# Performance work log

Measured on AMD Instinct MI355X. Metric: run time of the kernel, lower is better.

The kernel has to match this reference:

```python
import jax, jax.numpy as jnp
import numpy as np
import math

B, S, DM, H, F = 2, 2048, 1024, 16, 192  # F = head_dim init arg; per-head dim = F // 3
DH = F // 3
MAX_BIAS = 8.0


def _get_slopes(n):
    # faithful to ALiBiBias._get_slopes
    def pow2(n):
        start = 2.0 ** (-(2.0 ** (-(math.log2(n) - 3))))
        return [start * start ** i for i in range(n)]
    if math.log2(n).is_integer():
        return pow2(n)
    cp2 = 2 ** math.floor(math.log2(n))
    return pow2(cp2) + _get_slopes(2 * cp2)[0::2][: n - cp2]


def _rope_sin_cos(seq_len, dim):
    inv_freq = 1.0 / (10000.0 ** (jnp.arange(0, dim, 2, dtype=jnp.float32) / dim))
    freqs = jnp.outer(jnp.arange(seq_len, dtype=jnp.float32), inv_freq)  # [S, dim/2]
    # repeat(sin[:,None,:],2,axis=1).reshape(S,-1) == concat([sin,sin],-1)
    sin = jnp.concatenate([jnp.sin(freqs), jnp.sin(freqs)], axis=-1)  # [S, dim]
    cos = jnp.concatenate([jnp.cos(freqs), jnp.cos(freqs)], axis=-1)
    return sin, cos


def _rotate_half(x):
    x1, x2 = jnp.split(x, 2, axis=-1)
    return jnp.concatenate([-x2, x1], axis=-1)


def setup_inputs() -> dict:
    key = jax.random.key(0)
    kx, kq, ko = jax.random.split(key, 3)
    x = jax.random.normal(kx, (B, S, DM), dtype=jnp.float32)
    w_qkv = jax.random.normal(kq, (DM, H, F), dtype=jnp.float32) * (1.0 / math.sqrt(DM))
    b_qkv = jnp.zeros((H, F), dtype=jnp.float32)
    w_out = jax.random.normal(ko, (H, DH, DM), dtype=jnp.float32) * (1.0 / math.sqrt(H * DH))
    b_out = jnp.zeros((DM,), dtype=jnp.float32)
    return {"x": x, "w_qkv": w_qkv, "b_qkv": b_qkv, "w_out": w_out, "b_out": b_out}


def reference(x, w_qkv, b_qkv, w_out, b_out):
    b, s, dm = x.shape
    h, f = w_qkv.shape[1], w_qkv.shape[2]
    dh = f // 3
    # fused QKV projection: [B,S,H,F], then 3-way split on the feature axis
    qkv = jnp.einsum('bsd,dhf->bshf', x, w_qkv) + b_qkv
    q, k, v = jnp.split(qkv, 3, axis=-1)  # each [B,S,H,DH]
    # RoPE (rotate_half convention), broadcast over heads
    sin, cos = _rope_sin_cos(s, dh)
    sin, cos = sin[:, None, :], cos[:, None, :]  # [S,1,DH]
    q = q * cos + _rotate_half(q) * sin
    k = k * cos + _rotate_half(k) * sin
    # [B,H,S,DH]
    q = q.transpose(0, 2, 1, 3)
    k = k.transpose(0, 2, 1, 3)
    v = v.transpose(0, 2, 1, 3)
    # scores scaled by sqrt(head_dim init arg), as in the original non-flash path
    scores = jnp.einsum('bhqd,bhkd->bhqk', q, k) / jnp.sqrt(jnp.float32(f))
    # ALiBi bias
    slopes = jnp.asarray(_get_slopes(h), dtype=jnp.float32)  # [H]
    pos = jnp.arange(s, dtype=jnp.float32)
    rel = pos[None, :] - pos[:, None]  # j - i
    rel = jnp.where(rel > 0, 0.0, rel)
    alibi = rel[None, :, :] * slopes[:, None, None] * MAX_BIAS  # [H,S,S]
    scores = scores + alibi[None]  # [B,H,S,S]
    # causal mask
    causal = jnp.tril(jnp.ones((s, s), dtype=jnp.float32))
    scores = jnp.where(causal == 0, -1e9, scores)
    weights = jax.nn.softmax(scores, axis=-1)
    attn = jnp.einsum('bhqk,bhkd->bhqd', weights, v).transpose(0, 2, 1, 3)  # [B,S,H,DH]
    return jnp.einsum('bshd,hdm->bsm', attn, w_out) + b_out
```

## Files before the change

### kernel.cpp

```cpp
#include <hip/hip_runtime.h>
#include <math.h>

static constexpr int B_  = 2;
static constexpr int S_  = 2048;
static constexpr int H_  = 16;
static constexpr int DH_ = 64;
static constexpr float QSCALE2_ = 0.104117589f;
static constexpr float C8L2_    = 11.5415603f;

typedef __attribute__((ext_vector_type(8))) short short8;
typedef __attribute__((ext_vector_type(4))) float floatx4;

__device__ __forceinline__ float bf2f(unsigned short u) {
    union { unsigned int i; float f; } c; c.i = ((unsigned int)u) << 16; return c.f;
}
__device__ __forceinline__ unsigned short f2bf(float f) {
    union { float f; unsigned int i; } c; c.f = f;
    unsigned int x = c.i;
    unsigned int r = (x + 0x7fffu + ((x >> 16) & 1u)) >> 16;
    if ((x & 0x7f800000u) == 0x7f800000u) r = x >> 16;
    return (unsigned short)r;
}
__device__ __forceinline__ void load_lds16(const unsigned short* g, unsigned short* l) {
    __builtin_amdgcn_global_load_lds(
        (const __attribute__((address_space(1))) unsigned int*)g,
        (__attribute__((address_space(3))) unsigned int*)l, 16, 0, 0);
}

__global__ __launch_bounds__(256) void cvt_x(
    const float* __restrict__ in, unsigned short* __restrict__ out)
{
    const int i = blockIdx.x * 256 + threadIdx.x;
    const float4 v = reinterpret_cast<const float4*>(in)[i];
    ushort4 r;
    r.x = f2bf(v.x); r.y = f2bf(v.y); r.z = f2bf(v.z); r.w = f2bf(v.w);
    reinterpret_cast<ushort4*>(out)[i] = r;
}

template<int NN>
__global__ __launch_bounds__(256) void transcvt(
    const float* __restrict__ in, unsigned short* __restrict__ out)
{
    __shared__ float t[32][33];
    const int n0 = blockIdx.x * 32;
    const int k0 = blockIdx.y * 32;
    const int tn = threadIdx.x & 31, tk = threadIdx.x >> 5;
    #pragma unroll
    for (int i = 0; i < 4; ++i)
        t[tk + 8 * i][tn] = in[(size_t)(k0 + tk + 8 * i) * NN + n0 + tn];
    __syncthreads();
    #pragma unroll
    for (int i = 0; i < 4; ++i)
        out[(size_t)(n0 + tk + 8 * i) * 1024 + k0 + tn] = f2bf(t[tn][tk + 8 * i]);
}

template<int NW, int MODE>
__global__ __launch_bounds__(256) void gemm_mfma(
    const unsigned short* __restrict__ A, const unsigned short* __restrict__ BT,
    const float* __restrict__ bias,
    unsigned short* __restrict__ O0, unsigned short* __restrict__ O1,
    unsigned short* __restrict__ O2, float* __restrict__ Of)
{
    __shared__ unsigned short As[128 * 32];
    __shared__ unsigned short Bs[128 * 32];

    const int tid  = threadIdx.x;
    const int wave = tid >> 6;
    const int lane = tid & 63;
    const int quad = lane >> 4;
    const int lm   = lane & 15;
    const int wm = (wave >> 1) * 64;
    const int wn = (wave & 1) * 64;
    const int n0 = blockIdx.x * 128;
    const int m0 = blockIdx.y * 128;

    floatx4 acc[4][4] = {};

    const int sr = lane >> 2;
    const int sc = lane & 3;

    for (int k0 = 0; k0 < 1024; k0 += 32) {
        #pragma unroll
        for (int rep = 0; rep < 2; ++rep) {
            const int r = wave * 32 + rep * 16;
            load_lds16(A  + (size_t)(m0 + r + sr) * 1024 + k0 + sc * 8, &As[r * 32]);
            load_lds16(BT + (size_t)(n0 + r + sr) * 1024 + k0 + sc * 8, &Bs[r * 32]);
        }
        __syncthreads();
        short8 af[4], bf[4];
        #pragma unroll
        for (int i = 0; i < 4; ++i) {
            af[i] = *reinterpret_cast<const short8*>(&As[(wm + i * 16 + lm) * 32 + quad * 8]);
            bf[i] = *reinterpret_cast<const short8*>(&Bs[(wn + i * 16 + lm) * 32 + quad * 8]);
        }
        #pragma unroll
        for (int mi = 0; mi < 4; ++mi)
            #pragma unroll
            for (int ni = 0; ni < 4; ++ni)
                acc[mi][ni] = __builtin_amdgcn_mfma_f32_16x16x32_bf16(
                    af[mi], bf[ni], acc[mi][ni], 0, 0, 0);
        __syncthreads();
    }

    if (MODE == 1) {
        #pragma unroll
        for (int ni = 0; ni < 4; ++ni) {
            const int gn = n0 + wn + ni * 16 + lm;
            const float b = bias[gn];
            #pragma unroll
            for (int mi = 0; mi < 4; ++mi) {
                const int gm = m0 + wm + mi * 16 + quad * 4;
                #pragma unroll
                for (int r = 0; r < 4; ++r)
                    Of[(size_t)(gm + r) * 1024 + gn] = acc[mi][ni][r] + b;
            }
        }
    } else {
        const int nbase = n0 + wn;
        const int h   = nbase / 192;
        const int sec = (nbase - h * 192) >> 6;
        float bia[4];
        #pragma unroll
        for (int ni = 0; ni < 4; ++ni) bia[ni] = bias[nbase + ni * 16 + lm];
        unsigned short* Out = (sec == 0) ? O0 : ((sec == 1) ? O1 : O2);

        if (sec == 2) {
            #pragma unroll
            for (int mi = 0; mi < 4; ++mi) {
                const int m  = m0 + wm + mi * 16 + quad * 4;
                const int bb = m >> 11;
                const int s  = m & (S_ - 1);
                const size_t rowb = (size_t)(bb * H_ + h) * DH_;
                #pragma unroll
                for (int ni = 0; ni < 4; ++ni) {
                    const int d = ni * 16 + lm;
                    ushort4 w;
                    w.x = f2bf(acc[mi][ni][0] + bia[ni]);
                    w.y = f2bf(acc[mi][ni][1] + bia[ni]);
                    w.z = f2bf(acc[mi][ni][2] + bia[ni]);
                    w.w = f2bf(acc[mi][ni][3] + bia[ni]);
                    *reinterpret_cast<ushort4*>(&Out[(rowb + d) * S_ + s]) = w;
                }
            }
        } else {
            const float qscale = (sec == 0) ? QSCALE2_ : 1.0f;
            const float nlf = -13.287712379549449f / 32.0f;
            const float invf0 = exp2f((float)lm * nlf);
            const float invf1 = exp2f((float)(lm + 16) * nlf);
            #pragma unroll
            for (int mi = 0; mi < 4; ++mi) {
                #pragma unroll
                for (int r = 0; r < 4; ++r) {
                    const int m  = m0 + wm + mi * 16 + quad * 4 + r;
                    const int bb = m >> 11;
                    const int s  = m & (S_ - 1);
                    const size_t obase = ((size_t)(bb * H_ + h) * S_ + s) * DH_;
                    const float a0 = (float)s * invf0, a1 = (float)s * invf1;
                    const float sn0 = __sinf(a0), cs0 = __cosf(a0);
                    const float sn1 = __sinf(a1), cs1 = __cosf(a1);
                    #pragma unroll
                    for (int ni = 0; ni < 4; ++ni) {
                        const int d = ni * 16 + lm;
                        const float v = acc[mi][ni][r]     + bia[ni];
                        const float p = acc[mi][ni ^ 2][r] + bia[ni ^ 2];
                        const float cs = (ni & 1) ? cs1 : cs0;
                        const float sn = (ni & 1) ? sn1 : sn0;
                        float res = (d < 32) ? (v * cs - p * sn) : (v * cs + p * sn);
                        Out[obase + d] = f2bf(res * qscale);
                    }
                }
            }
        }
    }
}

static constexpr int KST = 68;
static constexpr int PST = 68;

__global__ __launch_bounds__(256) void flash_mfma(
    const unsigned short* __restrict__ Q, const unsigned short* __restrict__ K,
    const unsigned short* __restrict__ VT, unsigned short* __restrict__ Ao)
{
    __shared__ unsigned short Ks[2][64 * KST];
    __shared__ unsigned short VTs[2][64 * KST];
    __shared__ unsigned short Ps[4][16 * PST];

    const int bi = blockIdx.x;
    const int bh = bi & 31;
    const int pr = bi >> 5;
    const int h  = bh & 15;
    const int b  = bh >> 4;
    const int tid  = threadIdx.x;
    const int wave = tid >> 6;
    const int lane = tid & 63;
    const int quad = lane >> 4;
    const int lm   = lane & 15;
    const int srow = tid >> 2;
    const int sc8  = tid & 3;

    const unsigned short* Kg  = K  + (size_t)bh * S_ * DH_;
    const unsigned short* VTg = VT + (size_t)bh * DH_ * S_;

    const float slope2 = exp2f(-0.5f * (float)(h + 1)) * (8.0f * 1.44269504f);
    const float d64 = 64.0f * slope2;

    int   koff[4];
    float alb[4];
    #pragma unroll
    for (int t = 0; t < 4; ++t) {
        koff[t] = t * 16 + quad * 4 - wave * 16 - lm;
        alb[t]  = (float)koff[t] * slope2 - C8L2_;
    }

    unsigned short* Pw = &Ps[wave][0];

    for (int ph = 0; ph < 2; ++ph) {
        const int qt = ph ? pr : 31 - pr;

        const unsigned short* Qrow =
            Q + ((size_t)bh * S_ + (size_t)(qt * 64 + wave * 16 + lm)) * DH_;
        const short8 aq0 = *reinterpret_cast<const short8*>(Qrow + quad * 8);
        const short8 aq1 = *reinterpret_cast<const short8*>(Qrow + 32 + quad * 8);

        float crk[4];
        #pragma unroll
        for (int r = 0; r < 4; ++r)
            crk[r] = (float)r * slope2 - (float)qt * d64;

        float l_one = 0.0f;
        floatx4 acc_o[4] = {};

        short8 ka, kb, va, vb;
        {
            const unsigned short* kr = Kg + (size_t)srow * DH_ + sc8 * 8;
            ka = *reinterpret_cast<const short8*>(kr);
            kb = *reinterpret_cast<const short8*>(kr + 32);
            const unsigned short* vr = VTg + (size_t)srow * S_ + sc8 * 8;
            va = *reinterpret_cast<const short8*>(vr);
            vb = *reinterpret_cast<const short8*>(vr + 32);
        }
        *reinterpret_cast<short8*>(&Ks[0][srow * KST + sc8 * 8])       = ka;
        *reinterpret_cast<short8*>(&Ks[0][srow * KST + sc8 * 8 + 32])  = kb;
        *reinterpret_cast<short8*>(&VTs[0][srow * KST + sc8 * 8])      = va;
        *reinterpret_cast<short8*>(&VTs[0][srow * KST + sc8 * 8 + 32]) = vb;
        if (qt > 0) {
            const unsigned short* kr = Kg + (size_t)(64 + srow) * DH_ + sc8 * 8;
            ka = *reinterpret_cast<const short8*>(kr);
            kb = *reinterpret_cast<const short8*>(kr + 32);
            const unsigned short* vr = VTg + (size_t)srow * S_ + 64 + sc8 * 8;
            va = *reinterpret_cast<const short8*>(vr);
            vb = *reinterpret_cast<const short8*>(vr + 32);
        }
        __syncthreads();

        for (int kt = 0; kt <= qt; ++kt) {
            const int cur = kt & 1;

            if (kt < qt) {
                const int nxt = cur ^ 1;
                *reinterpret_cast<short8*>(&Ks[nxt][srow * KST + sc8 * 8])       = ka;
                *reinterpret_cast<short8*>(&Ks[nxt][srow * KST + sc8 * 8 + 32])  = kb;
                *reinterpret_cast<short8*>(&VTs[nxt][srow * KST + sc8 * 8])      = va;
                *reinterpret_cast<short8*>(&VTs[nxt][srow * KST + sc8 * 8 + 32]) = vb;
                if (kt + 1 < qt) {
                    const unsigned short* kr =
                        Kg + (size_t)((kt + 2) * 64 + srow) * DH_ + sc8 * 8;
                    ka = *reinterpret_cast<const short8*>(kr);
                    kb = *reinterpret_cast<const short8*>(kr + 32);
                    const unsigned short* vr =
                        VTg + (size_t)srow * S_ + (kt + 2) * 64 + sc8 * 8;
                    va = *reinterpret_cast<const short8*>(vr);
                    vb = *reinterpret_cast<const short8*>(vr + 32);
                }
            }

            floatx4 sacc[4] = {};
            #pragma unroll
            for (int t = 0; t < 4; ++t) {
                const short8 k0 = *reinterpret_cast<const short8*>(&Ks[cur][(t * 16 + lm) * KST + quad * 8]);
                const short8 k1 = *reinterpret_cast<const short8*>(&Ks[cur][(t * 16 + lm) * KST + 32 + quad * 8]);
                sacc[t] = __builtin_amdgcn_mfma_f32_16x16x32_bf16(k0, aq0, sacc[t], 0, 0, 0);
                sacc[t] = __builtin_amdgcn_mfma_f32_16x16x32_bf16(k1, aq1, sacc[t], 0, 0, 0);
            }

            const bool diag = (kt == qt);
            #pragma unroll
            for (int t = 0; t < 4; ++t) {
                float p[4];
                #pragma unroll
                for (int r = 0; r < 4; ++r) {
                    const float x = (sacc[t][r] + alb[t]) + crk[r];
                    float e;
                    asm("v_exp_f32 %0, %1" : "=v"(e) : "v"(x));
                    if (diag && (koff[t] + r) > 0) e = 0.0f;
                    p[r] = e;
                }
                l_one += (p[0] + p[1]) + (p[2] + p[3]);
                unsigned int lo, hi;
                asm("v_cvt_pk_bf16_f32 %0, %1, %2" : "=v"(lo) : "v"(p[0]), "v"(p[1]));
                asm("v_cvt_pk_bf16_f32 %0, %1, %2" : "=v"(hi) : "v"(p[2]), "v"(p[3]));
                uint2 w; w.x = lo; w.y = hi;
                *reinterpret_cast<uint2*>(&Pw[lm * PST + t * 16 + quad * 4]) = w;
            }
            #pragma unroll
            for (int r = 0; r < 4; ++r) crk[r] += d64;

            const short8 ap0 = *reinterpret_cast<const short8*>(&Pw[lm * PST + quad * 8]);
            const short8 ap1 = *reinterpret_cast<const short8*>(&Pw[lm * PST + 32 + quad * 8]);
            #pragma unroll
            for (int t = 0; t < 4; ++t) {
                const short8 v0 = *reinterpret_cast<const short8*>(&VTs[cur][(t * 16 + lm) * KST + quad * 8]);
                const short8 v1 = *reinterpret_cast<const short8*>(&VTs[cur][(t * 16 + lm) * KST + 32 + quad * 8]);
                acc_o[t] = __builtin_amdgcn_mfma_f32_16x16x32_bf16(ap0, v0, acc_o[t], 0, 0, 0);
                acc_o[t] = __builtin_amdgcn_mfma_f32_16x16x32_bf16(ap1, v1, acc_o[t], 0, 0, 0);
            }
            __syncthreads();
        }

        l_one += __shfl_xor(l_one, 16);
        l_one += __shfl_xor(l_one, 32);
        #pragma unroll
        for (int r = 0; r < 4; ++r) {
            const float lr = __shfl(l_one, quad * 4 + r);
            const float inv_l = 1.0f / lr;
            const int s = qt * 64 + wave * 16 + quad * 4 + r;
            const size_t obase = ((size_t)(b * S_ + s) * H_ + h) * DH_;
            #pragma unroll
            for (int t = 0; t < 4; ++t)
                Ao[obase + t * 16 + lm] = f2bf(acc_o[t][r] * inv_l);
        }
    }
}

extern "C" void kernel_launch(void* const* d_in, const int* in_sizes, int n_in,
                              void* d_out, int out_size, void* d_ws, size_t ws_size,
                              hipStream_t stream)
{
    const float *x = nullptr, *w_qkv = nullptr, *b_qkv = nullptr,
                *w_out = nullptr, *b_out = nullptr;
    for (int i = 0; i < n_in; ++i) {
        switch (in_sizes[i]) {
            case 4194304: x     = (const float*)d_in[i]; break;
            case 3145728: w_qkv = (const float*)d_in[i]; break;
            case 3072:    b_qkv = (const float*)d_in[i]; break;
            case 1048576: w_out = (const float*)d_in[i]; break;
            case 1024:    b_out = (const float*)d_in[i]; break;
        }
    }
    if (!x)     x     = (const float*)d_in[0];
    if (!w_qkv) w_qkv = (const float*)d_in[1];
    if (!b_qkv) b_qkv = (const float*)d_in[2];
    if (!w_out) w_out = (const float*)d_in[3];
    if (!b_out) b_out = (const float*)d_in[4];

    float* out = (float*)d_out;
    unsigned short* ws16 = (unsigned short*)d_ws;

    unsigned short* xb     = ws16;
    unsigned short* wqkvT  = ws16 + (size_t)4194304;
    unsigned short* woutT  = ws16 + (size_t)7340032;
    unsigned short* Qb     = ws16 + (size_t)8388608;
    unsigned short* Kb     = ws16 + (size_t)12582912;
    unsigned short* Vb     = ws16 + (size_t)16777216;
    unsigned short* Aob    = ws16 + (size_t)20971520;

    cvt_x<<<4096, 256, 0, stream>>>(x, xb);
    transcvt<3072><<<dim3(96, 32), 256, 0, stream>>>(w_qkv, wqkvT);
    transcvt<1024><<<dim3(32, 32), 256, 0, stream>>>(w_out, woutT);

    gemm_mfma<3072, 0><<<dim3(24, 32), 256, 0, stream>>>(
        xb, wqkvT, b_qkv, Qb, Kb, Vb, nullptr);
    flash_mfma<<<dim3(512), 256, 0, stream>>>(Qb, Kb, Vb, Aob);
    gemm_mfma<1024, 1><<<dim3(8, 32), 256, 0, stream>>>(
        Aob, woutT, b_out, nullptr, nullptr, nullptr, out);
}
```

Baseline: 199.4 us.

## Merge prep kernels, shrink output GEMM tile, add MFMA priority hints in flash

```diff
diff --git a/kernel.cpp b/kernel.cpp
--- a/kernel.cpp
+++ b/kernel.cpp
@@ -27,23 +27,31 @@
         (__attribute__((address_space(3))) unsigned int*)l, 16, 0, 0);
 }
 
-__global__ __launch_bounds__(256) void cvt_x(
-    const float* __restrict__ in, unsigned short* __restrict__ out)
-{
-    const int i = blockIdx.x * 256 + threadIdx.x;
-    const float4 v = reinterpret_cast<const float4*>(in)[i];
-    ushort4 r;
-    r.x = f2bf(v.x); r.y = f2bf(v.y); r.z = f2bf(v.z); r.w = f2bf(v.w);
-    reinterpret_cast<ushort4*>(out)[i] = r;
-}
-
-template<int NN>
-__global__ __launch_bounds__(256) void transcvt(
-    const float* __restrict__ in, unsigned short* __restrict__ out)
+__global__ __launch_bounds__(256) void prep(
+    const float* __restrict__ x,     unsigned short* __restrict__ xb,
+    const float* __restrict__ w_qkv, unsigned short* __restrict__ wqkvT,
+    const float* __restrict__ w_out, unsigned short* __restrict__ woutT)
 {
     __shared__ float t[32][33];
-    const int n0 = blockIdx.x * 32;
-    const int k0 = blockIdx.y * 32;
+    const int bid = blockIdx.x;
+    if (bid < 4096) {
+        const int i = bid * 256 + threadIdx.x;
+        const float4 v = reinterpret_cast<const float4*>(x)[i];
+        ushort4 r;
+        r.x = f2bf(v.x); r.y = f2bf(v.y); r.z = f2bf(v.z); r.w = f2bf(v.w);
+        reinterpret_cast<ushort4*>(xb)[i] = r;
+        return;
+    }
+    const float* in; unsigned short* out; int NN, bx, by;
+    if (bid < 7168) {
+        in = w_qkv; out = wqkvT; NN = 3072;
+        const int b2 = bid - 4096; bx = b2 % 96; by = b2 / 96;
+    } else {
+        in = w_out; out = woutT; NN = 1024;
+        const int b2 = bid - 7168; bx = b2 & 31; by = b2 >> 5;
+    }
+    const int n0 = bx * 32;
+    const int k0 = by * 32;
     const int tn = threadIdx.x & 31, tk = threadIdx.x >> 5;
     #pragma unroll
     for (int i = 0; i < 4; ++i)
@@ -54,12 +62,11 @@
         out[(size_t)(n0 + tk + 8 * i) * 1024 + k0 + tn] = f2bf(t[tn][tk + 8 * i]);
 }
 
-template<int NW, int MODE>
-__global__ __launch_bounds__(256) void gemm_mfma(
+__global__ __launch_bounds__(256) void gemm_qkv(
     const unsigned short* __restrict__ A, const unsigned short* __restrict__ BT,
     const float* __restrict__ bias,
     unsigned short* __restrict__ O0, unsigned short* __restrict__ O1,
-    unsigned short* __restrict__ O2, float* __restrict__ Of)
+    unsigned short* __restrict__ O2)
 {
     __shared__ unsigned short As[128 * 32];
     __shared__ unsigned short Bs[128 * 32];
@@ -102,74 +109,120 @@
         __syncthreads();
     }
 
-    if (MODE == 1) {
-        #pragma unroll
-        for (int ni = 0; ni < 4; ++ni) {
-            const int gn = n0 + wn + ni * 16 + lm;
-            const float b = bias[gn];
-            #pragma unroll
-            for (int mi = 0; mi < 4; ++mi) {
-                const int gm = m0 + wm + mi * 16 + quad * 4;
-                #pragma unroll
-                for (int r = 0; r < 4; ++r)
-                    Of[(size_t)(gm + r) * 1024 + gn] = acc[mi][ni][r] + b;
+    const int nbase = n0 + wn;
+    const int h   = nbase / 192;
+    const int sec = (nbase - h * 192) >> 6;
+    float bia[4];
+    #pragma unroll
+    for (int ni = 0; ni < 4; ++ni) bia[ni] = bias[nbase + ni * 16 + lm];
+    unsigned short* Out = (sec == 0) ? O0 : ((sec == 1) ? O1 : O2);
+
+    if (sec == 2) {
+        #pragma unroll
+        for (int mi = 0; mi < 4; ++mi) {
+            const int m  = m0 + wm + mi * 16 + quad * 4;
+            const int bb = m >> 11;
+            const int s  = m & (S_ - 1);
+            const size_t rowb = (size_t)(bb * H_ + h) * DH_;
+            #pragma unroll
+            for (int ni = 0; ni < 4; ++ni) {
+                const int d = ni * 16 + lm;
+                ushort4 w;
+                w.x = f2bf(acc[mi][ni][0] + bia[ni]);
+                w.y = f2bf(acc[mi][ni][1] + bia[ni]);
+                w.z = f2bf(acc[mi][ni][2] + bia[ni]);
+                w.w = f2bf(acc[mi][ni][3] + bia[ni]);
+                *reinterpret_cast<ushort4*>(&Out[(rowb + d) * S_ + s]) = w;
             }
         }
     } else {
-        const int nbase = n0 + wn;
-        const int h   = nbase / 192;
-        const int sec = (nbase - h * 192) >> 6;
-        float bia[4];
-        #pragma unroll
-        for (int ni = 0; ni < 4; ++ni) bia[ni] = bias[nbase + ni * 16 + lm];
-        unsigned short* Out = (sec == 0) ? O0 : ((sec == 1) ? O1 : O2);
-
-        if (sec == 2) {
-            #pragma unroll
-            for (int mi = 0; mi < 4; ++mi) {
-                const int m  = m0 + wm + mi * 16 + quad * 4;
+        const float qscale = (sec == 0) ? QSCALE2_ : 1.0f;
+        const float nlf = -13.287712379549449f / 32.0f;
+        const float invf0 = exp2f((float)lm * nlf);
+        const float invf1 = exp2f((float)(lm + 16) * nlf);
+        #pragma unroll
+        for (int mi = 0; mi < 4; ++mi) {
+            #pragma unroll
+            for (int r = 0; r < 4; ++r) {
+                const int m  = m0 + wm + mi * 16 + quad * 4 + r;
                 const int bb = m >> 11;
                 const int s  = m & (S_ - 1);
-                const size_t rowb = (size_t)(bb * H_ + h) * DH_;
+                const size_t obase = ((size_t)(bb * H_ + h) * S_ + s) * DH_;
+                const float a0 = (float)s * invf0, a1 = (float)s * invf1;
+                const float sn0 = __sinf(a0), cs0 = __cosf(a0);
+                const float sn1 = __sinf(a1), cs1 = __cosf(a1);
                 #pragma unroll
                 for (int ni = 0; ni < 4; ++ni) {
                     const int d = ni * 16 + lm;
-                    ushort4 w;
-                    w.x = f2bf(acc[mi][ni][0] + bia[ni]);
-                    w.y = f2bf(acc[mi][ni][1] + bia[ni]);
-                    w.z = f2bf(acc[mi][ni][2] + bia[ni]);
-                    w.w = f2bf(acc[mi][ni][3] + bia[ni]);
-                    *reinterpret_cast<ushort4*>(&Out[(rowb + d) * S_ + s]) = w;
+                    const float v = acc[mi][ni][r]     + bia[ni];
+                    const float p = acc[mi][ni ^ 2][r] + bia[ni ^ 2];
+                    const float cs = (ni & 1) ? cs1 : cs0;
+                    const float sn = (ni & 1) ? sn1 : sn0;
+                    float res = (d < 32) ? (v * cs - p * sn) : (v * cs + p * sn);
+                    Out[obase + d] = f2bf(res * qscale);
                 }
             }
-        } else {
-            const float qscale = (sec == 0) ? QSCALE2_ : 1.0f;
-            const float nlf = -13.287712379549449f / 32.0f;
-            const float invf0 = exp2f((float)lm * nlf);
-            const float invf1 = exp2f((float)(lm + 16) * nlf);
-            #pragma unroll
-            for (int mi = 0; mi < 4; ++mi) {
-                #pragma unroll
-                for (int r = 0; r < 4; ++r) {
-                    const int m  = m0 + wm + mi * 16 + quad * 4 + r;
-                    const int bb = m >> 11;
-                    const int s  = m & (S_ - 1);
-                    const size_t obase = ((size_t)(bb * H_ + h) * S_ + s) * DH_;
-                    const float a0 = (float)s * invf0, a1 = (float)s * invf1;
-                    const float sn0 = __sinf(a0), cs0 = __cosf(a0);
-                    const float sn1 = __sinf(a1), cs1 = __cosf(a1);
-                    #pragma unroll
-                    for (int ni = 0; ni < 4; ++ni) {
-                        const int d = ni * 16 + lm;
-                        const float v = acc[mi][ni][r]     + bia[ni];
-                        const float p = acc[mi][ni ^ 2][r] + bia[ni ^ 2];
-                        const float cs = (ni & 1) ? cs1 : cs0;
-                        const float sn = (ni & 1) ? sn1 : sn0;
-                        float res = (d < 32) ? (v * cs - p * sn) : (v * cs + p * sn);
-                        Out[obase + d] = f2bf(res * qscale);
-                    }
-                }
-            }
+        }
+    }
+}
+
+__global__ __launch_bounds__(256) void gemm_out(
+    const unsigned short* __restrict__ A, const unsigned short* __restrict__ BT,
+    const float* __restrict__ bias, float* __restrict__ Of)
+{
+    __shared__ unsigned short As[64 * 32];
+    __shared__ unsigned short Bs[128 * 32];
+
+    const int tid  = threadIdx.x;
+    const int wave = tid >> 6;
+    const int lane = tid & 63;
+    const int quad = lane >> 4;
+    const int lm   = lane & 15;
+    const int wm = (wave >> 1) * 32;
+    const int wn = (wave & 1) * 64;
+    const int n0 = blockIdx.x * 128;
+    const int m0 = blockIdx.y * 64;
+
+    floatx4 acc[2][4] = {};
+
+    const int sr = lane >> 2;
+    const int sc = lane & 3;
+
+    for (int k0 = 0; k0 < 1024; k0 += 32) {
+        load_lds16(A + (size_t)(m0 + wave * 16 + sr) * 1024 + k0 + sc * 8,
+                   &As[wave * 16 * 32]);
+        #pragma unroll
+        for (int rep = 0; rep < 2; ++rep) {
+            const int r = wave * 32 + rep * 16;
+            load_lds16(BT + (size_t)(n0 + r + sr) * 1024 + k0 + sc * 8, &Bs[r * 32]);
+        }
+        __syncthreads();
+        short8 af[2], bf[4];
+        #pragma unroll
+        for (int i = 0; i < 2; ++i)
+            af[i] = *reinterpret_cast<const short8*>(&As[(wm + i * 16 + lm) * 32 + quad * 8]);
+        #pragma unroll
+        for (int i = 0; i < 4; ++i)
+            bf[i] = *reinterpret_cast<const short8*>(&Bs[(wn + i * 16 + lm) * 32 + quad * 8]);
+        #pragma unroll
+        for (int mi = 0; mi < 2; ++mi)
+            #pragma unroll
+            for (int ni = 0; ni < 4; ++ni)
+                acc[mi][ni] = __builtin_amdgcn_mfma_f32_16x16x32_bf16(
+                    af[mi], bf[ni], acc[mi][ni], 0, 0, 0);
+        __syncthreads();
+    }
+
+    #pragma unroll
+    for (int ni = 0; ni < 4; ++ni) {
+        const int gn = n0 + wn + ni * 16 + lm;
+        const float b = bias[gn];
+        #pragma unroll
+        for (int mi = 0; mi < 2; ++mi) {
+            const int gm = m0 + wm + mi * 16 + quad * 4;
+            #pragma unroll
+            for (int r = 0; r < 4; ++r)
+                Of[(size_t)(gm + r) * 1024 + gn] = acc[mi][ni][r] + b;
         }
     }
 }
@@ -275,6 +328,7 @@
             }
 
             floatx4 sacc[4] = {};
+            __builtin_amdgcn_s_setprio(1);
             #pragma unroll
             for (int t = 0; t < 4; ++t) {
                 const short8 k0 = *reinterpret_cast<const short8*>(&Ks[cur][(t * 16 + lm) * KST + quad * 8]);
@@ -282,6 +336,7 @@
                 sacc[t] = __builtin_amdgcn_mfma_f32_16x16x32_bf16(k0, aq0, sacc[t], 0, 0, 0);
                 sacc[t] = __builtin_amdgcn_mfma_f32_16x16x32_bf16(k1, aq1, sacc[t], 0, 0, 0);
             }
+            __builtin_amdgcn_s_setprio(0);
 
             const bool diag = (kt == qt);
             #pragma unroll
@@ -307,6 +362,7 @@
 
             const short8 ap0 = *reinterpret_cast<const short8*>(&Pw[lm * PST + quad * 8]);
             const short8 ap1 = *reinterpret_cast<const short8*>(&Pw[lm * PST + 32 + quad * 8]);
+            __builtin_amdgcn_s_setprio(1);
             #pragma unroll
             for (int t = 0; t < 4; ++t) {
                 const short8 v0 = *reinterpret_cast<const short8*>(&VTs[cur][(t * 16 + lm) * KST + quad * 8]);
@@ -314,6 +370,7 @@
                 acc_o[t] = __builtin_amdgcn_mfma_f32_16x16x32_bf16(ap0, v0, acc_o[t], 0, 0, 0);
                 acc_o[t] = __builtin_amdgcn_mfma_f32_16x16x32_bf16(ap1, v1, acc_o[t], 0, 0, 0);
             }
+            __builtin_amdgcn_s_setprio(0);
             __syncthreads();
         }
 
@@ -364,13 +421,10 @@
     unsigned short* Vb     = ws16 + (size_t)16777216;
     unsigned short* Aob    = ws16 + (size_t)20971520;
 
-    cvt_x<<<4096, 256, 0, stream>>>(x, xb);
-    transcvt<3072><<<dim3(96, 32), 256, 0, stream>>>(w_qkv, wqkvT);
-    transcvt<1024><<<dim3(32, 32), 256, 0, stream>>>(w_out, woutT);
-
-    gemm_mfma<3072, 0><<<dim3(24, 32), 256, 0, stream>>>(
-        xb, wqkvT, b_qkv, Qb, Kb, Vb, nullptr);
+    prep<<<8192, 256, 0, stream>>>(x, xb, w_qkv, wqkvT, w_out, woutT);
+
+    gemm_qkv<<<dim3(24, 32), 256, 0, stream>>>(
+        xb, wqkvT, b_qkv, Qb, Kb, Vb);
     flash_mfma<<<dim3(512), 256, 0, stream>>>(Qb, Kb, Vb, Aob);
-    gemm_mfma<1024, 1><<<dim3(8, 32), 256, 0, stream>>>(
-        Aob, woutT, b_out, nullptr, nullptr, nullptr, out);
-}
+    gemm_out<<<dim3(8, 64), 256, 0, stream>>>(Aob, woutT, b_out, out);
+}
```

Result: faster. 192.9 us (-3.2%).
